# Kernel optimization log

Measured on AMD Instinct MI355X. Metric: run time of the kernel, lower is better.

Reference implementation:

```python
import jax, jax.numpy as jnp
import numpy as np

NC, NV = 1, 256
DE, D, DA = 512, 512, 512
KS = (2, 4, 4)
STRIDE = (2, 4, 4)
BLOCK = (4, 8, 8)
NHEAD = 8
NLAYERS = 2
PAD = -1
N_SLICE = STRIDE[0] * STRIDE[1] * STRIDE[2]  # 32


def _block_local_attention(x, wq, wk, wv, wo, block, n_head):
    # x: (b, d, T, H, W); non-overlapping block-local multi-head self-attention
    b, d, T, H, W = x.shape
    bt, bh, bw = block
    nt, nh, nw = T // bt, H // bh, W // bw
    L = bt * bh * bw
    da = wq.shape[1]
    hd = da // n_head
    # partition grid into blocks -> (b*nblocks, L, d)
    xs = x.transpose(0, 2, 3, 4, 1)                      # (b,T,H,W,d)
    xs = xs.reshape(b, nt, bt, nh, bh, nw, bw, d)
    xs = xs.transpose(0, 1, 3, 5, 2, 4, 6, 7).reshape(b * nt * nh * nw, L, d)
    q = (xs @ wq).reshape(-1, L, n_head, hd)
    k = (xs @ wk).reshape(-1, L, n_head, hd)
    v = (xs @ wv).reshape(-1, L, n_head, hd)
    scores = jnp.einsum('nqhd,nkhd->nhqk', q, k) / jnp.sqrt(jnp.float32(hd))
    attn = jax.nn.softmax(scores, axis=-1)
    o = jnp.einsum('nhqk,nkhd->nqhd', attn, v).reshape(-1, L, da)
    out = xs + o @ wo                                    # residual
    out = out.reshape(b, nt, nh, nw, bt, bh, bw, d)
    out = out.transpose(0, 1, 4, 2, 5, 3, 6, 7).reshape(b, T, H, W, d)
    return out.transpose(0, 4, 1, 2, 3)


def setup_inputs() -> dict:
    key = jax.random.key(0)
    ks = jax.random.split(key, 10)
    s = 0.02
    x = jax.random.randint(ks[0], (4, NC, 16, 64, 64), 0, NV)
    slice_idx = jax.random.randint(ks[1], (4,), 0, N_SLICE)
    conv_w = jax.random.normal(ks[2], (DE, NC * NV, *KS), jnp.float32) * s
    conv_b = jax.random.normal(ks[3], (DE,), jnp.float32) * s
    slice_emb = jax.random.normal(ks[4], (N_SLICE, DE), jnp.float32) * s
    proj_w = jax.random.normal(ks[5], (D, DE), jnp.float32) * s
    attn_wq = jax.random.normal(ks[6], (NLAYERS, D, DA), jnp.float32) * s
    attn_wk = jax.random.normal(ks[7], (NLAYERS, D, DA), jnp.float32) * s
    attn_wv = jax.random.normal(ks[8], (NLAYERS, D, DA), jnp.float32) * s
    attn_wo = jax.random.normal(ks[9], (NLAYERS, DA, D), jnp.float32) * s
    return {"x": x, "slice_idx": slice_idx, "conv_w": conv_w, "conv_b": conv_b,
            "slice_emb": slice_emb, "proj_w": proj_w, "attn_wq": attn_wq,
            "attn_wk": attn_wk, "attn_wv": attn_wv, "attn_wo": attn_wo}


def reference(x, slice_idx, conv_w, conv_b, slice_emb, proj_w,
              attn_wq, attn_wk, attn_wv, attn_wo):
    mask = x == PAD                                        # (b,nc,T,H,W)
    xt = jnp.where(mask, 0, x)
    oh = jax.nn.one_hot(xt, NV, dtype=jnp.float32)         # (b,nc,T,H,W,nv)
    oh = oh * (~mask)[..., None].astype(jnp.float32)
    b, nc, T, H, W, nv = oh.shape
    h = oh.transpose(0, 1, 5, 2, 3, 4).reshape(b, nc * nv, T, H, W)
    h = jax.lax.conv_general_dilated(h, conv_w, STRIDE, 'VALID',
                                     dimension_numbers=('NCDHW', 'OIDHW', 'NCDHW'))
    h = h + conv_b[None, :, None, None, None]
    h = h + slice_emb[slice_idx][:, :, None, None, None]
    h = jnp.einsum('bcthw,dc->bdthw', h, proj_w)           # 1x1x1 conv, no bias
    for i in range(NLAYERS):
        h = _block_local_attention(h, attn_wq[i], attn_wk[i], attn_wv[i],
                                   attn_wo[i], BLOCK, NHEAD)
    return h
```

## Files before the change

kernel.cpp:

```cpp
#include <hip/hip_runtime.h>
#include <hip/hip_bf16.h>

typedef unsigned short u16x8 __attribute__((ext_vector_type(8)));
typedef unsigned int u32x4 __attribute__((ext_vector_type(4)));
typedef __bf16 bf16x8 __attribute__((ext_vector_type(8)));
typedef float f32x4 __attribute__((ext_vector_type(4)));
typedef float f32x16 __attribute__((ext_vector_type(16)));

#define NTAP 32
#define NROWS 8192

__device__ inline unsigned short bf16bits(float f) {
  __hip_bfloat16 hb = __float2bfloat16(f);
  return __builtin_bit_cast(unsigned short, hb);
}
__device__ inline unsigned int pk2(float lo, float hi) {
  return (unsigned int)bf16bits(lo) | ((unsigned int)bf16bits(hi) << 16);
}
__device__ inline float bf2f(unsigned short u) {
  return __builtin_bit_cast(float, (unsigned int)u << 16);
}

__global__ void k_prep(const float* __restrict__ conv_w, const float* __restrict__ proj_w,
                       const float* __restrict__ wq, const float* __restrict__ wk,
                       const float* __restrict__ wv, const float* __restrict__ wo,
                       unsigned short* __restrict__ wTb, unsigned short* __restrict__ Wb) {
  __shared__ float tile[64][65];
  int bid = blockIdx.x;
  int t = threadIdx.x;
  if (bid < 1024) {
    int vt0 = (bid & 127) * 64, de0 = (bid >> 7) * 64;
#pragma unroll
    for (int p = 0; p < 16; p++) {
      int r = p * 4 + (t >> 6), c = t & 63;
      tile[r][c] = conv_w[(size_t)(de0 + r) * 8192 + vt0 + c];
    }
    __syncthreads();
#pragma unroll
    for (int p = 0; p < 16; p++) {
      int r = p * 4 + (t >> 6), c = t & 63;
      wTb[(size_t)(vt0 + r) * 512 + de0 + c] = bf16bits(tile[c][r]);
    }
  } else {
    int wid2 = bid - 1024;
    int mat = wid2 >> 6, rem = wid2 & 63;
    int n0 = (rem & 7) * 64, k0 = (rem >> 3) * 64;
    unsigned short* dst = Wb + (size_t)mat * 262144;
    if (mat == 0) {
#pragma unroll
      for (int p = 0; p < 16; p++) {
        int r = p * 4 + (t >> 6), c = t & 63;
        dst[(size_t)(n0 + r) * 512 + k0 + c] = bf16bits(proj_w[(size_t)(n0 + r) * 512 + k0 + c]);
      }
    } else {
      int idx = mat - 1, comp = idx & 3, L = idx >> 2;
      const float* srcs[4] = {wq, wk, wv, wo};
      const float* src = srcs[comp] + (size_t)L * 262144;
#pragma unroll
      for (int p = 0; p < 16; p++) {
        int r = p * 4 + (t >> 6), c = t & 63;
        tile[r][c] = src[(size_t)(k0 + r) * 512 + n0 + c];
      }
      __syncthreads();
#pragma unroll
      for (int p = 0; p < 16; p++) {
        int r = p * 4 + (t >> 6), c = t & 63;
        dst[(size_t)(n0 + r) * 512 + k0 + c] = bf16bits(tile[c][r]);
      }
    }
  }
}

__global__ void k_embed(const int* __restrict__ x, const int* __restrict__ slice_idx,
                        const unsigned short* __restrict__ wTb, const float* __restrict__ conv_b,
                        const float* __restrict__ slice_emb, unsigned short* __restrict__ H0b) {
  int tid = threadIdx.x;
  int g = tid >> 6, l = tid & 63;
  int r = blockIdx.x * 4 + g;
  int blk = r >> 8, ll = r & 255;
  int bw = blk & 1, bh = (blk >> 1) & 1, bt = (blk >> 2) & 1, b = blk >> 3;
  int lw = ll & 7, lh = (ll >> 3) & 7, lt = ll >> 6;
  int t = bt * 4 + lt, h = bh * 8 + lh, w = bw * 8 + lw;

  __shared__ int toks[4][NTAP];
  if (l < NTAP) {
    int kt = l >> 4, kh = (l >> 2) & 3, kw = l & 3;
    toks[g][l] = x[((b * 16 + (2 * t + kt)) * 64 + (4 * h + kh)) * 64 + (4 * w + kw)];
  }
  __syncthreads();
  int sl = slice_idx[b];
  float4 cb0 = *(const float4*)&conv_b[l * 8];
  float4 cb1 = *(const float4*)&conv_b[l * 8 + 4];
  float4 se0 = *(const float4*)&slice_emb[sl * 512 + l * 8];
  float4 se1 = *(const float4*)&slice_emb[sl * 512 + l * 8 + 4];
  float acc[8] = {cb0.x + se0.x, cb0.y + se0.y, cb0.z + se0.z, cb0.w + se0.w,
                  cb1.x + se1.x, cb1.y + se1.y, cb1.z + se1.z, cb1.w + se1.w};
  for (int tap = 0; tap < NTAP; tap++) {
    int v = toks[g][tap];
    if (v >= 0) {
      u16x8 wv = *(const u16x8*)&wTb[(size_t)(v * NTAP + tap) * 512 + l * 8];
#pragma unroll
      for (int j = 0; j < 8; j++) acc[j] += bf2f(wv[j]);
    }
  }
  u16x8 o;
#pragma unroll
  for (int j = 0; j < 8; j++) o[j] = bf16bits(acc[j]);
  *(u16x8*)&H0b[(size_t)r * 512 + l * 8] = o;
}

template <int WM, bool RES>
__global__ void __launch_bounds__(256)
k_gemm_mfma(const unsigned short* __restrict__ A, const unsigned short* __restrict__ B,
            float* __restrict__ Cf, unsigned short* __restrict__ Cb,
            unsigned short* __restrict__ Vt) {
  struct ABb { unsigned short As[128 * 64]; unsigned short Bs[128 * 64]; };
  union SMu { ABb ab; unsigned short T[64][136]; };
  __shared__ __align__(16) SMu sm;
  unsigned short* As = sm.ab.As;
  unsigned short* Bs = sm.ab.Bs;
  int m0 = blockIdx.x * 128, n0 = blockIdx.y * 128;
  int tid = threadIdx.x;
  int lane = tid & 63, wid = tid >> 6;
  int wr = wid >> 1, wc = wid & 1;
  int l15 = lane & 15, lgrp = lane >> 4;
  int srow = tid >> 3, sx = tid & 7;
  f32x4 acc[4][4] = {};
  for (int k0 = 0; k0 < 512; k0 += 64) {
    u16x8 ra[4], rb[4];
#pragma unroll
    for (int i = 0; i < 4; i++) {
      int row = i * 32 + srow;
      int c = sx ^ (row & 7);
      ra[i] = *(const u16x8*)&A[(size_t)(m0 + row) * 512 + k0 + c * 8];
      rb[i] = *(const u16x8*)&B[(size_t)(n0 + row) * 512 + k0 + c * 8];
    }
    __syncthreads();
#pragma unroll
    for (int i = 0; i < 4; i++) {
      int row = i * 32 + srow;
      *(u16x8*)&As[row * 64 + sx * 8] = ra[i];
      *(u16x8*)&Bs[row * 64 + sx * 8] = rb[i];
    }
    __syncthreads();
#pragma unroll
    for (int kk = 0; kk < 2; kk++) {
      bf16x8 a[4], b[4];
#pragma unroll
      for (int m = 0; m < 4; m++) {
        int row = wr * 64 + m * 16 + l15;
        int xx = (kk * 4 + lgrp) ^ (row & 7);
        a[m] = __builtin_bit_cast(bf16x8, *(const u16x8*)&As[row * 64 + xx * 8]);
      }
#pragma unroll
      for (int n = 0; n < 4; n++) {
        int row = wc * 64 + n * 16 + l15;
        int xx = (kk * 4 + lgrp) ^ (row & 7);
        b[n] = __builtin_bit_cast(bf16x8, *(const u16x8*)&Bs[row * 64 + xx * 8]);
      }
#pragma unroll
      for (int m = 0; m < 4; m++)
#pragma unroll
        for (int n = 0; n < 4; n++)
          acc[m][n] = __builtin_amdgcn_mfma_f32_16x16x32_bf16(a[m], b[n], acc[m][n], 0, 0, 0);
    }
  }
  if (WM == 2 && n0 >= 1024) {
    __syncthreads();
#pragma unroll
    for (int p = 0; p < 2; p++) {
      if (wc == p) {
#pragma unroll
        for (int m = 0; m < 4; m++)
#pragma unroll
          for (int n = 0; n < 4; n++)
#pragma unroll
            for (int r = 0; r < 4; r++)
              sm.T[n * 16 + l15][wr * 64 + m * 16 + lgrp * 4 + r] = bf16bits(acc[m][n][r]);
      }
      __syncthreads();
      int c = tid >> 2, rcb = tid & 3;
#pragma unroll
      for (int it = 0; it < 4; it++) {
        int rc = it * 4 + rcb;
        *(u16x8*)&Vt[(size_t)(n0 - 1024 + p * 64 + c) * 8192 + m0 + rc * 8] =
            *(const u16x8*)&sm.T[c][rc * 8];
      }
      if (p == 0) __syncthreads();
    }
    return;
  }
#pragma unroll
  for (int m = 0; m < 4; m++) {
#pragma unroll
    for (int n = 0; n < 4; n++) {
      int gcol = n0 + wc * 64 + n * 16 + l15;
#pragma unroll
      for (int r = 0; r < 4; r++) {
        int grow = m0 + wr * 64 + m * 16 + lgrp * 4 + r;
        float v = acc[m][n][r];
        if (WM == 1) {
          if (RES) v += Cf[(size_t)grow * 512 + gcol];
          Cf[(size_t)grow * 512 + gcol] = v;
          Cb[(size_t)grow * 512 + gcol] = bf16bits(v);
        } else {
          Cb[(size_t)grow * 1024 + gcol] = bf16bits(v);
        }
      }
    }
  }
}

__global__ void __launch_bounds__(256)
k_attn_mfma(const unsigned short* __restrict__ QKb, const unsigned short* __restrict__ Vt,
            unsigned short* __restrict__ O16) {
  __shared__ __align__(16) unsigned short Ks[256 * 64];
  __shared__ __align__(16) unsigned short Vs[64 * 256];
  int xg = blockIdx.x;
  int bid = xg >> 4, head = (xg >> 1) & 7, qh = xg & 1;
  int r0 = bid * 256;
  int tid = threadIdx.x, lane = tid & 63, wid = tid >> 6;
  {
    int key = tid >> 3, j = tid & 7;
#pragma unroll
    for (int p = 0; p < 8; p++) {
      int k2 = key + p * 32;
      u16x8 v = *(const u16x8*)&QKb[(size_t)(r0 + k2) * 1024 + 512 + head * 64 + j * 8];
      *(u16x8*)&Ks[k2 * 64 + ((j ^ (k2 & 7)) * 8)] = v;
    }
    int dv = tid >> 2, sg = tid & 3;
    const unsigned short* src = &Vt[(size_t)(head * 64 + dv) * 8192 + r0 + sg * 64];
#pragma unroll
    for (int c = 0; c < 8; c++) {
      u16x8 v = *(const u16x8*)&src[c * 8];
      int ch = sg * 8 + c;
      *(u16x8*)&Vs[dv * 256 + ((ch ^ (dv & 7)) * 8)] = v;
    }
  }
  int l31 = lane & 31, hi = lane >> 5;
  int q = r0 + qh * 128 + wid * 32 + l31;
  bf16x8 qfrag[4];
#pragma unroll
  for (int s = 0; s < 4; s++)
    qfrag[s] = __builtin_bit_cast(
        bf16x8, *(const u16x8*)&QKb[(size_t)q * 1024 + head * 64 + s * 16 + hi * 8]);
  __syncthreads();

  f32x16 oacc[2] = {};
  float mx = -1e30f, lsum = 0.f;

  for (int kt = 0; kt < 8; kt++) {
    bf16x8 kfrag[4];
    int key = kt * 32 + l31;
#pragma unroll
    for (int s = 0; s < 4; s++) {
      int j = s * 2 + hi;
      kfrag[s] = __builtin_bit_cast(bf16x8, *(const u16x8*)&Ks[key * 64 + ((j ^ (key & 7)) * 8)]);
    }
    f32x16 sacc = {};
#pragma unroll
    for (int s = 0; s < 4; s++)
      sacc = __builtin_amdgcn_mfma_f32_32x32x16_bf16(kfrag[s], qfrag[s], sacc, 0, 0, 0);
    float tmax = sacc[0];
#pragma unroll
    for (int r = 1; r < 16; r++) tmax = fmaxf(tmax, sacc[r]);
    tmax = fmaxf(tmax, __shfl_xor(tmax, 32, 64));
    float mn = fmaxf(mx, tmax);
    float sc = __expf((mx - mn) * 0.125f);
    float p[16], ts = 0.f;
#pragma unroll
    for (int r = 0; r < 16; r++) {
      p[r] = __expf((sacc[r] - mn) * 0.125f);
      ts += p[r];
    }
    ts += __shfl_xor(ts, 32, 64);
    lsum = lsum * sc + ts;
    mx = mn;
#pragma unroll
    for (int dvt = 0; dvt < 2; dvt++)
#pragma unroll
      for (int r = 0; r < 16; r++) oacc[dvt][r] *= sc;
#pragma unroll
    for (int st = 0; st < 2; st++) {
      unsigned int Aw = pk2(p[st * 8 + 0], p[st * 8 + 1]);
      unsigned int Bw = pk2(p[st * 8 + 2], p[st * 8 + 3]);
      unsigned int Cw = pk2(p[st * 8 + 4], p[st * 8 + 5]);
      unsigned int Dw = pk2(p[st * 8 + 6], p[st * 8 + 7]);
      asm volatile("v_permlane32_swap_b32 %0, %1" : "+v"(Aw), "+v"(Cw));
      asm volatile("v_permlane32_swap_b32 %0, %1" : "+v"(Bw), "+v"(Dw));
      u32x4 fw = {Aw, Bw, Cw, Dw};
      bf16x8 pfrag = __builtin_bit_cast(bf16x8, fw);
#pragma unroll
      for (int dvt = 0; dvt < 2; dvt++) {
        int dv = dvt * 32 + l31;
        int ch = kt * 4 + st * 2 + hi;
        bf16x8 vfrag = __builtin_bit_cast(
            bf16x8, *(const u16x8*)&Vs[dv * 256 + ((ch ^ (dv & 7)) * 8)]);
        oacc[dvt] = __builtin_amdgcn_mfma_f32_32x32x16_bf16(vfrag, pfrag, oacc[dvt], 0, 0, 0);
      }
    }
  }
  float inv = 1.f / lsum;
  size_t rowb = (size_t)q * 512 + head * 64;
#pragma unroll
  for (int dvt = 0; dvt < 2; dvt++)
#pragma unroll
    for (int r = 0; r < 16; r += 2) {
      int dv = dvt * 32 + (r & 3) + 8 * (r >> 2) + 4 * hi;
      unsigned int po = pk2(oacc[dvt][r] * inv, oacc[dvt][r + 1] * inv);
      *(unsigned int*)&O16[rowb + dv] = po;
    }
}

__global__ void k_writeout(const float* __restrict__ H, float* __restrict__ out) {
  __shared__ float t[512][33];
  int bp = blockIdx.x;
  int d0 = blockIdx.y * 32;
  int tid = threadIdx.x;
  int base_row = bp * 512;
#pragma unroll
  for (int i = 0; i < 16; i++) {
    int id = i * 256 + tid;
    int r = id >> 3, c = id & 7;
    float4 v = *(const float4*)&H[(size_t)(base_row + r) * 512 + d0 + c * 4];
    t[r][c * 4 + 0] = v.x;
    t[r][c * 4 + 1] = v.y;
    t[r][c * 4 + 2] = v.z;
    t[r][c * 4 + 3] = v.w;
  }
  __syncthreads();
  int b = bp >> 2, bt = (bp >> 1) & 1, bh = bp & 1;
  int w = tid & 15, lh = (tid >> 4) & 7, ltl = tid >> 7;
  int lw = w & 7, bw = w >> 3;
#pragma unroll
  for (int dd = 0; dd < 32; dd++) {
#pragma unroll
    for (int s = 0; s < 2; s++) {
      int lt = s * 2 + ltl;
      int pos = bw * 256 + lt * 64 + lh * 8 + lw;
      out[((size_t)(b * 512 + d0 + dd) * 8 + bt * 4 + lt) * 256 + (bh * 8 + lh) * 16 + w] =
          t[pos][dd];
    }
  }
}

extern "C" void kernel_launch(void* const* d_in, const int* in_sizes, int n_in,
                              void* d_out, int out_size, void* d_ws, size_t ws_size,
                              hipStream_t stream) {
  const int* x = (const int*)d_in[0];
  const int* slice_idx = (const int*)d_in[1];
  const float* conv_w = (const float*)d_in[2];
  const float* conv_b = (const float*)d_in[3];
  const float* slice_emb = (const float*)d_in[4];
  const float* proj_w = (const float*)d_in[5];
  const float* wq = (const float*)d_in[6];
  const float* wk = (const float*)d_in[7];
  const float* wv = (const float*)d_in[8];
  const float* wo = (const float*)d_in[9];
  float* out = (float*)d_out;

  float* ws = (float*)d_ws;
  unsigned short* wTb = (unsigned short*)ws;
  float* H = ws + 4194304;
  unsigned short* H0b = (unsigned short*)(ws + 8388608);
  unsigned short* Hb = (unsigned short*)(ws + 10485760);
  unsigned short* Ob16 = (unsigned short*)(ws + 12582912);
  unsigned short* QKb = (unsigned short*)(ws + 14680064);
  unsigned short* Vt = (unsigned short*)(ws + 18874368);
  unsigned short* Wb = (unsigned short*)(ws + 20971520);

  k_prep<<<1600, 256, 0, stream>>>(conv_w, proj_w, wq, wk, wv, wo, wTb, Wb);
  k_embed<<<2048, 256, 0, stream>>>(x, slice_idx, wTb, conv_b, slice_emb, H0b);
  k_gemm_mfma<1, false><<<dim3(64, 4), 256, 0, stream>>>(H0b, Wb, H, Hb, nullptr);

  for (int L = 0; L < 2; L++) {
    k_gemm_mfma<2, false><<<dim3(64, 12), 256, 0, stream>>>(
        Hb, Wb + (size_t)262144 * (1 + 4 * L), nullptr, QKb, Vt);
    k_attn_mfma<<<512, 256, 0, stream>>>(QKb, Vt, Ob16);
    k_gemm_mfma<1, true><<<dim3(64, 4), 256, 0, stream>>>(
        Ob16, Wb + (size_t)262144 * (4 + 4 * L), H, Hb, nullptr);
  }
  k_writeout<<<dim3(16, 16), 256, 0, stream>>>(H, out);
}
```

Measured before the change: 265.8 us.

## Prefetch next GEMM K-tile into registers and give each attention block both query halves

The GEMM kernel now loads the next 64-wide K slice into registers right after the shared-memory stores, so the global loads overlap with the MFMA compute on the current tile. The attention kernel now assigns each block a full (block, head) pair and has every wave process two 32-query groups. Each K/V tile staged in shared memory is therefore reused across twice as many queries, and the grid is halved. In exchange, attention blocks roughly double their register pressure and only 256 blocks launch, which may leave some of the GPU's compute units idle.

```diff
diff --git a/kernel.cpp b/kernel.cpp
--- a/kernel.cpp
+++ b/kernel.cpp
@@ -126,15 +126,15 @@
   int l15 = lane & 15, lgrp = lane >> 4;
   int srow = tid >> 3, sx = tid & 7;
   f32x4 acc[4][4] = {};
+  u16x8 ra[4], rb[4];
+#pragma unroll
+  for (int i = 0; i < 4; i++) {
+    int row = i * 32 + srow;
+    int c = sx ^ (row & 7);
+    ra[i] = *(const u16x8*)&A[(size_t)(m0 + row) * 512 + c * 8];
+    rb[i] = *(const u16x8*)&B[(size_t)(n0 + row) * 512 + c * 8];
+  }
   for (int k0 = 0; k0 < 512; k0 += 64) {
-    u16x8 ra[4], rb[4];
-#pragma unroll
-    for (int i = 0; i < 4; i++) {
-      int row = i * 32 + srow;
-      int c = sx ^ (row & 7);
-      ra[i] = *(const u16x8*)&A[(size_t)(m0 + row) * 512 + k0 + c * 8];
-      rb[i] = *(const u16x8*)&B[(size_t)(n0 + row) * 512 + k0 + c * 8];
-    }
     __syncthreads();
 #pragma unroll
     for (int i = 0; i < 4; i++) {
@@ -143,6 +143,15 @@
       *(u16x8*)&Bs[row * 64 + sx * 8] = rb[i];
     }
     __syncthreads();
+    if (k0 + 64 < 512) {
+#pragma unroll
+      for (int i = 0; i < 4; i++) {
+        int row = i * 32 + srow;
+        int c = sx ^ (row & 7);
+        ra[i] = *(const u16x8*)&A[(size_t)(m0 + row) * 512 + k0 + 64 + c * 8];
+        rb[i] = *(const u16x8*)&B[(size_t)(n0 + row) * 512 + k0 + 64 + c * 8];
+      }
+    }
 #pragma unroll
     for (int kk = 0; kk < 2; kk++) {
       bf16x8 a[4], b[4];
@@ -216,8 +225,7 @@
             unsigned short* __restrict__ O16) {
   __shared__ __align__(16) unsigned short Ks[256 * 64];
   __shared__ __align__(16) unsigned short Vs[64 * 256];
-  int xg = blockIdx.x;
-  int bid = xg >> 4, head = (xg >> 1) & 7, qh = xg & 1;
+  int bid = blockIdx.x >> 3, head = blockIdx.x & 7;
   int r0 = bid * 256;
   int tid = threadIdx.x, lane = tid & 63, wid = tid >> 6;
   {
@@ -238,16 +246,19 @@
     }
   }
   int l31 = lane & 31, hi = lane >> 5;
-  int q = r0 + qh * 128 + wid * 32 + l31;
-  bf16x8 qfrag[4];
-#pragma unroll
-  for (int s = 0; s < 4; s++)
-    qfrag[s] = __builtin_bit_cast(
-        bf16x8, *(const u16x8*)&QKb[(size_t)q * 1024 + head * 64 + s * 16 + hi * 8]);
+  int qb = wid * 64;
+  bf16x8 qfrag[2][4];
+#pragma unroll
+  for (int g = 0; g < 2; g++)
+#pragma unroll
+    for (int s = 0; s < 4; s++)
+      qfrag[g][s] = __builtin_bit_cast(
+          bf16x8, *(const u16x8*)&QKb[(size_t)(r0 + qb + g * 32 + l31) * 1024 + head * 64 +
+                                      s * 16 + hi * 8]);
   __syncthreads();
 
-  f32x16 oacc[2] = {};
-  float mx = -1e30f, lsum = 0.f;
+  f32x16 oacc[2][2] = {};
+  float mx[2] = {-1e30f, -1e30f}, lsum[2] = {0.f, 0.f};
 
   for (int kt = 0; kt < 8; kt++) {
     bf16x8 kfrag[4];
@@ -257,59 +268,65 @@
       int j = s * 2 + hi;
       kfrag[s] = __builtin_bit_cast(bf16x8, *(const u16x8*)&Ks[key * 64 + ((j ^ (key & 7)) * 8)]);
     }
-    f32x16 sacc = {};
-#pragma unroll
-    for (int s = 0; s < 4; s++)
-      sacc = __builtin_amdgcn_mfma_f32_32x32x16_bf16(kfrag[s], qfrag[s], sacc, 0, 0, 0);
-    float tmax = sacc[0];
-#pragma unroll
-    for (int r = 1; r < 16; r++) tmax = fmaxf(tmax, sacc[r]);
-    tmax = fmaxf(tmax, __shfl_xor(tmax, 32, 64));
-    float mn = fmaxf(mx, tmax);
-    float sc = __expf((mx - mn) * 0.125f);
-    float p[16], ts = 0.f;
-#pragma unroll
-    for (int r = 0; r < 16; r++) {
-      p[r] = __expf((sacc[r] - mn) * 0.125f);
-      ts += p[r];
-    }
-    ts += __shfl_xor(ts, 32, 64);
-    lsum = lsum * sc + ts;
-    mx = mn;
+#pragma unroll
+    for (int g = 0; g < 2; g++) {
+      f32x16 sacc = {};
+#pragma unroll
+      for (int s = 0; s < 4; s++)
+        sacc = __builtin_amdgcn_mfma_f32_32x32x16_bf16(kfrag[s], qfrag[g][s], sacc, 0, 0, 0);
+      float tmax = sacc[0];
+#pragma unroll
+      for (int r = 1; r < 16; r++) tmax = fmaxf(tmax, sacc[r]);
+      tmax = fmaxf(tmax, __shfl_xor(tmax, 32, 64));
+      float mn = fmaxf(mx[g], tmax);
+      float sc = __expf((mx[g] - mn) * 0.125f);
+      float p[16], ts = 0.f;
+#pragma unroll
+      for (int r = 0; r < 16; r++) {
+        p[r] = __expf((sacc[r] - mn) * 0.125f);
+        ts += p[r];
+      }
+      ts += __shfl_xor(ts, 32, 64);
+      lsum[g] = lsum[g] * sc + ts;
+      mx[g] = mn;
+#pragma unroll
+      for (int dvt = 0; dvt < 2; dvt++)
+#pragma unroll
+        for (int r = 0; r < 16; r++) oacc[g][dvt][r] *= sc;
+#pragma unroll
+      for (int st = 0; st < 2; st++) {
+        unsigned int Aw = pk2(p[st * 8 + 0], p[st * 8 + 1]);
+        unsigned int Bw = pk2(p[st * 8 + 2], p[st * 8 + 3]);
+        unsigned int Cw = pk2(p[st * 8 + 4], p[st * 8 + 5]);
+        unsigned int Dw = pk2(p[st * 8 + 6], p[st * 8 + 7]);
+        asm volatile("v_permlane32_swap_b32 %0, %1" : "+v"(Aw), "+v"(Cw));
+        asm volatile("v_permlane32_swap_b32 %0, %1" : "+v"(Bw), "+v"(Dw));
+        u32x4 fw = {Aw, Bw, Cw, Dw};
+        bf16x8 pfrag = __builtin_bit_cast(bf16x8, fw);
+#pragma unroll
+        for (int dvt = 0; dvt < 2; dvt++) {
+          int dv = dvt * 32 + l31;
+          int ch = kt * 4 + st * 2 + hi;
+          bf16x8 vfrag = __builtin_bit_cast(
+              bf16x8, *(const u16x8*)&Vs[dv * 256 + ((ch ^ (dv & 7)) * 8)]);
+          oacc[g][dvt] = __builtin_amdgcn_mfma_f32_32x32x16_bf16(vfrag, pfrag, oacc[g][dvt], 0, 0, 0);
+        }
+      }
+    }
+  }
+#pragma unroll
+  for (int g = 0; g < 2; g++) {
+    float inv = 1.f / lsum[g];
+    size_t rowb = (size_t)(r0 + qb + g * 32 + l31) * 512 + head * 64;
 #pragma unroll
     for (int dvt = 0; dvt < 2; dvt++)
 #pragma unroll
-      for (int r = 0; r < 16; r++) oacc[dvt][r] *= sc;
-#pragma unroll
-    for (int st = 0; st < 2; st++) {
-      unsigned int Aw = pk2(p[st * 8 + 0], p[st * 8 + 1]);
-      unsigned int Bw = pk2(p[st * 8 + 2], p[st * 8 + 3]);
-      unsigned int Cw = pk2(p[st * 8 + 4], p[st * 8 + 5]);
-      unsigned int Dw = pk2(p[st * 8 + 6], p[st * 8 + 7]);
-      asm volatile("v_permlane32_swap_b32 %0, %1" : "+v"(Aw), "+v"(Cw));
-      asm volatile("v_permlane32_swap_b32 %0, %1" : "+v"(Bw), "+v"(Dw));
-      u32x4 fw = {Aw, Bw, Cw, Dw};
-      bf16x8 pfrag = __builtin_bit_cast(bf16x8, fw);
-#pragma unroll
-      for (int dvt = 0; dvt < 2; dvt++) {
-        int dv = dvt * 32 + l31;
-        int ch = kt * 4 + st * 2 + hi;
-        bf16x8 vfrag = __builtin_bit_cast(
-            bf16x8, *(const u16x8*)&Vs[dv * 256 + ((ch ^ (dv & 7)) * 8)]);
-        oacc[dvt] = __builtin_amdgcn_mfma_f32_32x32x16_bf16(vfrag, pfrag, oacc[dvt], 0, 0, 0);
-      }
-    }
-  }
-  float inv = 1.f / lsum;
-  size_t rowb = (size_t)q * 512 + head * 64;
-#pragma unroll
-  for (int dvt = 0; dvt < 2; dvt++)
-#pragma unroll
-    for (int r = 0; r < 16; r += 2) {
-      int dv = dvt * 32 + (r & 3) + 8 * (r >> 2) + 4 * hi;
-      unsigned int po = pk2(oacc[dvt][r] * inv, oacc[dvt][r + 1] * inv);
-      *(unsigned int*)&O16[rowb + dv] = po;
-    }
+      for (int r = 0; r < 16; r += 2) {
+        int dv = dvt * 32 + (r & 3) + 8 * (r >> 2) + 4 * hi;
+        unsigned int po = pk2(oacc[g][dvt][r] * inv, oacc[g][dvt][r + 1] * inv);
+        *(unsigned int*)&O16[rowb + dv] = po;
+      }
+  }
 }
 
 __global__ void k_writeout(const float* __restrict__ H, float* __restrict__ out) {
@@ -376,7 +393,7 @@
   for (int L = 0; L < 2; L++) {
     k_gemm_mfma<2, false><<<dim3(64, 12), 256, 0, stream>>>(
         Hb, Wb + (size_t)262144 * (1 + 4 * L), nullptr, QKb, Vt);
-    k_attn_mfma<<<512, 256, 0, stream>>>(QKb, Vt, Ob16);
+    k_attn_mfma<<<256, 256, 0, stream>>>(QKb, Vt, Ob16);
     k_gemm_mfma<1, true><<<dim3(64, 4), 256, 0, stream>>>(
         Ob16, Wb + (size_t)262144 * (4 + 4 * L), H, Hb, nullptr);
   }
```

After: 247.1 us. 7.1% less time.
